# Kernel optimization log

Measured on AMD Instinct MI355X. Metric: run time of the kernel, lower is better.

## Reference

```python
import jax, jax.numpy as jnp
import numpy as np

N_NODES = 50000


def gcn_conv(x, edge_index, W, b, n_nodes):
    # Linear transform first (as in PyG GCNConv), then normalized aggregation
    xw = x @ W  # [N, out]
    src, dst = edge_index[0], edge_index[1]
    loops = jnp.arange(n_nodes, dtype=src.dtype)
    s = jnp.concatenate([src, loops])  # add self-loops
    d = jnp.concatenate([dst, loops])
    deg = jax.ops.segment_sum(jnp.ones_like(s, dtype=xw.dtype), d, num_segments=n_nodes)
    dinv = jnp.where(deg > 0, jax.lax.rsqrt(deg), 0.0)
    norm = dinv[s] * dinv[d]  # [E+N]
    msg = xw[s] * norm[:, None]  # gather + scale
    out = jax.ops.segment_sum(msg, d, num_segments=n_nodes)  # scatter-add
    return out + b


def setup_inputs() -> dict:
    key = jax.random.key(0)
    k1, k2, k3, k4 = jax.random.split(key, 4)
    in_dim, hidden = 128, 128
    n_edges = 625000
    x = jax.random.normal(k1, (N_NODES, in_dim), dtype=jnp.float32)
    edge_index = jax.random.randint(k2, (2, n_edges), 0, N_NODES, dtype=jnp.int64)
    # glorot-ish scale
    W1 = jax.random.normal(k3, (in_dim, hidden), dtype=jnp.float32) * (1.0 / np.sqrt(in_dim))
    b1 = jnp.zeros((hidden,), dtype=jnp.float32)
    W2 = jax.random.normal(k4, (hidden, hidden), dtype=jnp.float32) * (1.0 / np.sqrt(hidden))
    b2 = jnp.zeros((hidden,), dtype=jnp.float32)
    return {"x": x, "edge_index": edge_index, "W1": W1, "b1": b1, "W2": W2, "b2": b2}


def reference(x, edge_index, W1, b1, W2, b2):
    n = x.shape[0]
    h = gcn_conv(x, edge_index, W1, b1, n)
    h = jax.nn.relu(h)
    # dropout(p=0.3) is identity in eval mode
    h = gcn_conv(h, edge_index, W2, b2, n)
    return jax.nn.relu(h)
```

## Files before the change

kernel.cpp:

```cpp
#include <hip/hip_runtime.h>
#include <hip/hip_bf16.h>

#define NNODES 50000
#define BKT 64
#define LP 136
#define NXCD 8
#define NPX 6250

typedef short bf16x8 __attribute__((ext_vector_type(8)));
typedef float f32x4 __attribute__((ext_vector_type(4)));

__device__ __forceinline__ unsigned short f2bf_rn(float f) {
    unsigned int u = __float_as_uint(f);
    return (unsigned short)((u + 0x7fffu + ((u >> 16) & 1u)) >> 16);
}
__device__ __forceinline__ float bf_lo(unsigned int u) { return __uint_as_float(u << 16); }
__device__ __forceinline__ float bf_hi(unsigned int u) { return __uint_as_float(u & 0xffff0000u); }


__global__ __launch_bounds__(256) void k_wt(const float* __restrict__ W1,
                                            const float* __restrict__ W2,
                                            unsigned short* __restrict__ WT1,
                                            unsigned short* __restrict__ WT2,
                                            int* __restrict__ cnt, int N) {
    __shared__ float tile[128 * 129];
    int b = blockIdx.x, t = threadIdx.x;
    if (b < 2) {
        const float* W = b ? W2 : W1;
        unsigned short* WT = b ? WT2 : WT1;
        for (int idx = t; idx < 128 * 128; idx += 256)
            tile[(idx >> 7) * 129 + (idx & 127)] = W[idx];
        __syncthreads();
        for (int idx = t; idx < 128 * 128; idx += 256) {
            int c = idx >> 7, k = idx & 127;
            WT[c * 128 + k] = f2bf_rn(tile[k * 129 + c]);
        }
    } else {
        int i = (b - 2) * 256 + t;
        if (i < N) cnt[i] = 0;
    }
}


__device__ __forceinline__ void gather_accum(const unsigned int* __restrict__ xwb,
                                             const int* __restrict__ cnt,
                                             const unsigned short* __restrict__ bp,
                                             int degc, int lane,
                                             float& ax, float& ay) {
    float px = 0.f, py = 0.f;
    int j = 0;
    for (; j + 8 <= degc; j += 8) {
        int4 q = *(const int4*)&bp[j];
        int s0 = q.x & 0xffff, s1 = (int)((unsigned)q.x >> 16);
        int s2 = q.y & 0xffff, s3 = (int)((unsigned)q.y >> 16);
        int s4 = q.z & 0xffff, s5 = (int)((unsigned)q.z >> 16);
        int s6 = q.w & 0xffff, s7 = (int)((unsigned)q.w >> 16);
        unsigned int u0 = xwb[(size_t)s0 * 64 + lane];
        unsigned int u1 = xwb[(size_t)s1 * 64 + lane];
        unsigned int u2 = xwb[(size_t)s2 * 64 + lane];
        unsigned int u3 = xwb[(size_t)s3 * 64 + lane];
        unsigned int u4 = xwb[(size_t)s4 * 64 + lane];
        unsigned int u5 = xwb[(size_t)s5 * 64 + lane];
        unsigned int u6 = xwb[(size_t)s6 * 64 + lane];
        unsigned int u7 = xwb[(size_t)s7 * 64 + lane];
        float w0 = rsqrtf((float)cnt[s0] + 1.0f), w1 = rsqrtf((float)cnt[s1] + 1.0f);
        float w2 = rsqrtf((float)cnt[s2] + 1.0f), w3 = rsqrtf((float)cnt[s3] + 1.0f);
        float w4 = rsqrtf((float)cnt[s4] + 1.0f), w5 = rsqrtf((float)cnt[s5] + 1.0f);
        float w6 = rsqrtf((float)cnt[s6] + 1.0f), w7 = rsqrtf((float)cnt[s7] + 1.0f);
        ax = fmaf(bf_lo(u0), w0, ax);  ay = fmaf(bf_hi(u0), w0, ay);
        px = fmaf(bf_lo(u1), w1, px);  py = fmaf(bf_hi(u1), w1, py);
        ax = fmaf(bf_lo(u2), w2, ax);  ay = fmaf(bf_hi(u2), w2, ay);
        px = fmaf(bf_lo(u3), w3, px);  py = fmaf(bf_hi(u3), w3, py);
        ax = fmaf(bf_lo(u4), w4, ax);  ay = fmaf(bf_hi(u4), w4, ay);
        px = fmaf(bf_lo(u5), w5, px);  py = fmaf(bf_hi(u5), w5, py);
        ax = fmaf(bf_lo(u6), w6, ax);  ay = fmaf(bf_hi(u6), w6, ay);
        px = fmaf(bf_lo(u7), w7, px);  py = fmaf(bf_hi(u7), w7, py);
    }
    if (j + 4 <= degc) {
        int2 q = *(const int2*)&bp[j];
        int s0 = q.x & 0xffff, s1 = (int)((unsigned)q.x >> 16);
        int s2 = q.y & 0xffff, s3 = (int)((unsigned)q.y >> 16);
        unsigned int u0 = xwb[(size_t)s0 * 64 + lane];
        unsigned int u1 = xwb[(size_t)s1 * 64 + lane];
        unsigned int u2 = xwb[(size_t)s2 * 64 + lane];
        unsigned int u3 = xwb[(size_t)s3 * 64 + lane];
        float w0 = rsqrtf((float)cnt[s0] + 1.0f), w1 = rsqrtf((float)cnt[s1] + 1.0f);
        float w2 = rsqrtf((float)cnt[s2] + 1.0f), w3 = rsqrtf((float)cnt[s3] + 1.0f);
        ax = fmaf(bf_lo(u0), w0, ax);  ay = fmaf(bf_hi(u0), w0, ay);
        px = fmaf(bf_lo(u1), w1, px);  py = fmaf(bf_hi(u1), w1, py);
        ax = fmaf(bf_lo(u2), w2, ax);  ay = fmaf(bf_hi(u2), w2, ay);
        px = fmaf(bf_lo(u3), w3, px);  py = fmaf(bf_hi(u3), w3, py);
        j += 4;
    }
    for (; j < degc; ++j) {
        int s = bp[j];
        float wv = rsqrtf((float)cnt[s] + 1.0f);
        unsigned int u = xwb[(size_t)s * 64 + lane];
        ax = fmaf(bf_lo(u), wv, ax);
        ay = fmaf(bf_hi(u), wv, ay);
    }
    ax += px;
    ay += py;
}


__global__ __launch_bounds__(256) void k_gemmbucket(const float* __restrict__ X,
                                                    const unsigned short* __restrict__ WT,
                                                    unsigned short* __restrict__ Yb, int n,
                                                    const int* __restrict__ src,
                                                    const int* __restrict__ dst,
                                                    int* __restrict__ cnt,
                                                    unsigned short* __restrict__ bkt,
                                                    int E, int EBTOT) {
    __shared__ unsigned short Ep[64 * LP];
    int t = threadIdx.x;
    if ((int)blockIdx.x < EBTOT) {
        int g = blockIdx.x & (NXCD - 1);
        int kk = blockIdx.x >> 3;
        int lo = g * NPX;
        int SLOTS = E >> 2;
        int idx = kk * 256 + t;
        if (idx < SLOTS) {
            int4 d4 = ((const int4*)dst)[idx];
            int e0 = idx << 2;
            if ((unsigned)(d4.x - lo) < (unsigned)NPX) {
                int pos = atomicAdd(&cnt[d4.x], 1);
                if (pos < BKT) bkt[(size_t)d4.x * BKT + pos] = (unsigned short)src[e0];
            }
            if ((unsigned)(d4.y - lo) < (unsigned)NPX) {
                int pos = atomicAdd(&cnt[d4.y], 1);
                if (pos < BKT) bkt[(size_t)d4.y * BKT + pos] = (unsigned short)src[e0 + 1];
            }
            if ((unsigned)(d4.z - lo) < (unsigned)NPX) {
                int pos = atomicAdd(&cnt[d4.z], 1);
                if (pos < BKT) bkt[(size_t)d4.z * BKT + pos] = (unsigned short)src[e0 + 2];
            }
            if ((unsigned)(d4.w - lo) < (unsigned)NPX) {
                int pos = atomicAdd(&cnt[d4.w], 1);
                if (pos < BKT) bkt[(size_t)d4.w * BKT + pos] = (unsigned short)src[e0 + 3];
            }
        }
        if (kk == 0 && t < (E & 3)) {
            int e = (E & ~3) + t;
            int d = dst[e];
            if ((unsigned)(d - lo) < (unsigned)NPX) {
                int pos = atomicAdd(&cnt[d], 1);
                if (pos < BKT) bkt[(size_t)d * BKT + pos] = (unsigned short)src[e];
            }
        }
        return;
    }
    int gb = blockIdx.x - EBTOT;
    int lane = t & 63, w = t >> 6;
    int m = lane & 15, quad = lane >> 4;
    int base = gb * 64 + w * 16;
    int row = min(base + m, n - 1);

    bf16x8 a[4];
#pragma unroll
    for (int kt = 0; kt < 4; ++kt) {
        const float* pa = &X[(size_t)row * 128 + kt * 32 + quad * 8];
        float4 v0 = *(const float4*)pa;
        float4 v1 = *(const float4*)(pa + 4);
        a[kt][0] = (short)f2bf_rn(v0.x); a[kt][1] = (short)f2bf_rn(v0.y);
        a[kt][2] = (short)f2bf_rn(v0.z); a[kt][3] = (short)f2bf_rn(v0.w);
        a[kt][4] = (short)f2bf_rn(v1.x); a[kt][5] = (short)f2bf_rn(v1.y);
        a[kt][6] = (short)f2bf_rn(v1.z); a[kt][7] = (short)f2bf_rn(v1.w);
    }

    f32x4 acc[8];
#pragma unroll
    for (int i = 0; i < 8; ++i) acc[i] = f32x4{0.f, 0.f, 0.f, 0.f};
#pragma unroll
    for (int kt = 0; kt < 4; ++kt) {
        int ko = kt * 32 + quad * 8;
#pragma unroll
        for (int ct = 0; ct < 8; ++ct) {
            bf16x8 b = *(const bf16x8*)&WT[(ct * 16 + m) * 128 + ko];
            acc[ct] = __builtin_amdgcn_mfma_f32_16x16x32_bf16(a[kt], b, acc[ct], 0, 0, 0);
        }
    }

    unsigned short* ep = &Ep[w * 16 * LP];
#pragma unroll
    for (int ct = 0; ct < 8; ++ct)
#pragma unroll
        for (int r = 0; r < 4; ++r)
            ep[(quad * 4 + r) * LP + ct * 16 + m] = f2bf_rn(acc[ct][r]);
    __syncthreads();
    int rr = lane & 15, cc = lane >> 4;
    int orow = base + rr;
    if (orow < n) {
#pragma unroll
        for (int i2 = 0; i2 < 4; ++i2)
            ((uint4*)&Yb[(size_t)orow * 128])[cc * 4 + i2] =
                *(const uint4*)&ep[rr * LP + (cc * 4 + i2) * 8];
    }
}


__global__ __launch_bounds__(1024, 2) void k_aggemm(const unsigned int* __restrict__ xw1,
                                                    const int* __restrict__ cnt,
                                                    const unsigned short* __restrict__ bkt,
                                                    const float* __restrict__ bias,
                                                    const unsigned short* __restrict__ WT2,
                                                    unsigned short* __restrict__ xw2, int n) {
    __shared__ unsigned short Wl[128 * LP];
    __shared__ unsigned short At[16 * LP];
    int t = threadIdx.x, lane = t & 63, w = t >> 6;
    int base = blockIdx.x * 16;

    for (int idx = t; idx < 128 * 16; idx += 1024) {
        int r = idx >> 4, c8 = (idx & 15) << 3;
        *(uint4*)&Wl[r * LP + c8] = *(const uint4*)&WT2[r * 128 + c8];
    }

    int i = min(base + w, n - 1);
    int deg = cnt[i];
    int degc = min(deg, BKT);
    float di = rsqrtf((float)deg + 1.0f);
    unsigned int v0 = xw1[(size_t)i * 64 + lane];
    float ax = di * bf_lo(v0), ay = di * bf_hi(v0);
    gather_accum(xw1, cnt, &bkt[(size_t)i * BKT], degc, lane, ax, ay);
    float bx = bias[lane * 2], by = bias[lane * 2 + 1];
    ax = fmaxf(fmaf(di, ax, bx), 0.0f);
    ay = fmaxf(fmaf(di, ay, by), 0.0f);
    ((unsigned int*)&At[w * LP])[lane] = (unsigned)f2bf_rn(ax) | ((unsigned)f2bf_rn(ay) << 16);
    __syncthreads();

    int m = lane & 15, quad = lane >> 4;
    f32x4 acc = f32x4{0.f, 0.f, 0.f, 0.f};
    if (w < 8) {
        bf16x8 a[4];
#pragma unroll
        for (int kt = 0; kt < 4; ++kt)
            a[kt] = *(const bf16x8*)&At[m * LP + kt * 32 + quad * 8];
#pragma unroll
        for (int kt = 0; kt < 4; ++kt) {
            bf16x8 b = *(const bf16x8*)&Wl[(w * 16 + m) * LP + kt * 32 + quad * 8];
            acc = __builtin_amdgcn_mfma_f32_16x16x32_bf16(a[kt], b, acc, 0, 0, 0);
        }
    }
    __syncthreads();
    if (w < 8) {
#pragma unroll
        for (int r = 0; r < 4; ++r)
            At[(quad * 4 + r) * LP + w * 16 + m] = f2bf_rn(acc[r]);
    }
    __syncthreads();
    if (t < 256) {
        int row = t >> 4, q = t & 15;
        int orow = base + row;
        if (orow < n)
            *(uint4*)&xw2[(size_t)orow * 128 + q * 8] = *(const uint4*)&At[row * LP + q * 8];
    }
}


__global__ __launch_bounds__(256) void k_agg(const unsigned int* __restrict__ xwb,
                                             const int* __restrict__ cnt,
                                             const unsigned short* __restrict__ bkt,
                                             const float* __restrict__ bias,
                                             float* __restrict__ out, int n) {
    int lane = threadIdx.x & 63;
    int i = (blockIdx.x * 256 + threadIdx.x) >> 6;
    if (i >= n) return;
    int deg = cnt[i];
    int degc = min(deg, BKT);
    float di = rsqrtf((float)deg + 1.0f);
    unsigned int v0 = xwb[(size_t)i * 64 + lane];
    float ax = di * bf_lo(v0), ay = di * bf_hi(v0);
    gather_accum(xwb, cnt, &bkt[(size_t)i * BKT], degc, lane, ax, ay);
    float bx = bias[lane * 2], by = bias[lane * 2 + 1];
    ax = fmaxf(fmaf(di, ax, bx), 0.0f);
    ay = fmaxf(fmaf(di, ay, by), 0.0f);
    ((float2*)out)[(size_t)i * 64 + lane] = make_float2(ax, ay);
}


extern "C" void kernel_launch(void* const* d_in, const int* in_sizes, int n_in,
                              void* d_out, int out_size, void* d_ws, size_t ws_size,
                              hipStream_t stream) {
    const float* x  = (const float*)d_in[0];
    const int*   ei = (const int*)d_in[1];
    const float* W1 = (const float*)d_in[2];
    const float* b1 = (const float*)d_in[3];
    const float* W2 = (const float*)d_in[4];
    const float* b2 = (const float*)d_in[5];
    float* out = (float*)d_out;

    const int N = NNODES;
    const int E = in_sizes[1] / 2;
    const int* src = ei;
    const int* dst = ei + E;

    char* p = (char*)d_ws;
    size_t off = 0;
    auto take = [&](size_t bytes) -> void* {
        void* r = p + off;
        off = (off + bytes + 255) & ~(size_t)255;
        return r;
    };
    int* cnt = (int*)take((size_t)N * 4);
    unsigned short* bkt = (unsigned short*)take((size_t)N * BKT * 2);
    unsigned short* w1t = (unsigned short*)take(128 * 128 * 2);
    unsigned short* w2t = (unsigned short*)take(128 * 128 * 2);
    unsigned short* xw1 = (unsigned short*)take((size_t)N * 128 * 2);
    unsigned short* xw2 = (unsigned short*)take((size_t)N * 128 * 2);

    const int NB = (N + 255) / 256;
    const int SLOTS = E / 4;
    const int NBG = (SLOTS + 255) / 256;
    const int EBTOT = NBG * NXCD;
    const int GB = (N + 63) / 64;

    k_wt<<<2 + NB, 256, 0, stream>>>(W1, W2, w1t, w2t, cnt, N);
    k_gemmbucket<<<EBTOT + GB, 256, 0, stream>>>(x, w1t, xw1, N, src, dst, cnt, bkt, E, EBTOT);
    k_aggemm<<<(N + 15) / 16, 1024, 0, stream>>>((const unsigned int*)xw1, cnt, bkt,
                                                 b1, w2t, xw2, N);
    k_agg<<<(N * 64 + 255) / 256, 256, 0, stream>>>((const unsigned int*)xw2, cnt, bkt,
                                                    b2, out, N);
}
```

Measured before the change: 209.9 us.

## Prescale layer-2 features by source norm, persistent agg loops, simpler edge bucketing

Edge bucketing no longer filters by XCD node range. Each bucketing block now handles 8 edges per thread with vector loads and is interleaved 1-in-3 with GEMM blocks. The layer-1 aggregate+GEMM kernel becomes a persistent grid-stride loop that reads W2 straight from global memory instead of staging it in LDS, and it multiplies outputs by the row's dinv. Because xw2 is prescaled by source degree norm, the final aggregation does plain sums without per-neighbour cnt loads and rsqrt, and runs as a persistent grid. This removes dependent cnt gathers in layer 2 and the per-block W2 LDS staging, at the cost of more atomic contention across XCDs and W2 reloads from cache.

```diff
diff --git a/kernel.cpp b/kernel.cpp
--- a/kernel.cpp
+++ b/kernel.cpp
@@ -4,8 +4,9 @@
 #define NNODES 50000
 #define BKT 64
 #define LP 136
-#define NXCD 8
-#define NPX 6250
+#define EPT 8
+#define AGG_BLOCKS 2048
+#define AGE_BLOCKS 512
 
 typedef short bf16x8 __attribute__((ext_vector_type(8)));
 typedef float f32x4 __attribute__((ext_vector_type(4)));
@@ -104,6 +105,60 @@
 }
 
 
+__device__ __forceinline__ void gather_sum(const unsigned int* __restrict__ xwb,
+                                           const unsigned short* __restrict__ bp,
+                                           int degc, int lane,
+                                           float& ax, float& ay) {
+    float px = 0.f, py = 0.f;
+    int j = 0;
+    for (; j + 8 <= degc; j += 8) {
+        int4 q = *(const int4*)&bp[j];
+        int s0 = q.x & 0xffff, s1 = (int)((unsigned)q.x >> 16);
+        int s2 = q.y & 0xffff, s3 = (int)((unsigned)q.y >> 16);
+        int s4 = q.z & 0xffff, s5 = (int)((unsigned)q.z >> 16);
+        int s6 = q.w & 0xffff, s7 = (int)((unsigned)q.w >> 16);
+        unsigned int u0 = xwb[(size_t)s0 * 64 + lane];
+        unsigned int u1 = xwb[(size_t)s1 * 64 + lane];
+        unsigned int u2 = xwb[(size_t)s2 * 64 + lane];
+        unsigned int u3 = xwb[(size_t)s3 * 64 + lane];
+        unsigned int u4 = xwb[(size_t)s4 * 64 + lane];
+        unsigned int u5 = xwb[(size_t)s5 * 64 + lane];
+        unsigned int u6 = xwb[(size_t)s6 * 64 + lane];
+        unsigned int u7 = xwb[(size_t)s7 * 64 + lane];
+        ax += bf_lo(u0);  ay += bf_hi(u0);
+        px += bf_lo(u1);  py += bf_hi(u1);
+        ax += bf_lo(u2);  ay += bf_hi(u2);
+        px += bf_lo(u3);  py += bf_hi(u3);
+        ax += bf_lo(u4);  ay += bf_hi(u4);
+        px += bf_lo(u5);  py += bf_hi(u5);
+        ax += bf_lo(u6);  ay += bf_hi(u6);
+        px += bf_lo(u7);  py += bf_hi(u7);
+    }
+    if (j + 4 <= degc) {
+        int2 q = *(const int2*)&bp[j];
+        int s0 = q.x & 0xffff, s1 = (int)((unsigned)q.x >> 16);
+        int s2 = q.y & 0xffff, s3 = (int)((unsigned)q.y >> 16);
+        unsigned int u0 = xwb[(size_t)s0 * 64 + lane];
+        unsigned int u1 = xwb[(size_t)s1 * 64 + lane];
+        unsigned int u2 = xwb[(size_t)s2 * 64 + lane];
+        unsigned int u3 = xwb[(size_t)s3 * 64 + lane];
+        ax += bf_lo(u0);  ay += bf_hi(u0);
+        px += bf_lo(u1);  py += bf_hi(u1);
+        ax += bf_lo(u2);  ay += bf_hi(u2);
+        px += bf_lo(u3);  py += bf_hi(u3);
+        j += 4;
+    }
+    for (; j < degc; ++j) {
+        int s = bp[j];
+        unsigned int u = xwb[(size_t)s * 64 + lane];
+        ax += bf_lo(u);
+        ay += bf_hi(u);
+    }
+    ax += px;
+    ay += py;
+}
+
+
 __global__ __launch_bounds__(256) void k_gemmbucket(const float* __restrict__ X,
                                                     const unsigned short* __restrict__ WT,
                                                     unsigned short* __restrict__ Yb, int n,
@@ -111,46 +166,42 @@
                                                     const int* __restrict__ dst,
                                                     int* __restrict__ cnt,
                                                     unsigned short* __restrict__ bkt,
-                                                    int E, int EBTOT) {
+                                                    int E, int EB8) {
     __shared__ unsigned short Ep[64 * LP];
     int t = threadIdx.x;
-    if ((int)blockIdx.x < EBTOT) {
-        int g = blockIdx.x & (NXCD - 1);
-        int kk = blockIdx.x >> 3;
-        int lo = g * NPX;
-        int SLOTS = E >> 2;
-        int idx = kk * 256 + t;
-        if (idx < SLOTS) {
-            int4 d4 = ((const int4*)dst)[idx];
-            int e0 = idx << 2;
-            if ((unsigned)(d4.x - lo) < (unsigned)NPX) {
-                int pos = atomicAdd(&cnt[d4.x], 1);
-                if (pos < BKT) bkt[(size_t)d4.x * BKT + pos] = (unsigned short)src[e0];
+    int b = blockIdx.x;
+    int region = EB8 * 3;
+    if (b < region && (b % 3) == 0) {
+        int bid = b / 3;
+        int e0 = bid * 256 * EPT + t * EPT;
+        if (e0 + EPT <= E) {
+            int4 sa = *(const int4*)&src[e0];
+            int4 sb = *(const int4*)&src[e0 + 4];
+            int4 da = *(const int4*)&dst[e0];
+            int4 db = *(const int4*)&dst[e0 + 4];
+            int p;
+            p = atomicAdd(&cnt[da.x], 1); if (p < BKT) bkt[(size_t)da.x * BKT + p] = (unsigned short)sa.x;
+            p = atomicAdd(&cnt[da.y], 1); if (p < BKT) bkt[(size_t)da.y * BKT + p] = (unsigned short)sa.y;
+            p = atomicAdd(&cnt[da.z], 1); if (p < BKT) bkt[(size_t)da.z * BKT + p] = (unsigned short)sa.z;
+            p = atomicAdd(&cnt[da.w], 1); if (p < BKT) bkt[(size_t)da.w * BKT + p] = (unsigned short)sa.w;
+            p = atomicAdd(&cnt[db.x], 1); if (p < BKT) bkt[(size_t)db.x * BKT + p] = (unsigned short)sb.x;
+            p = atomicAdd(&cnt[db.y], 1); if (p < BKT) bkt[(size_t)db.y * BKT + p] = (unsigned short)sb.y;
+            p = atomicAdd(&cnt[db.z], 1); if (p < BKT) bkt[(size_t)db.z * BKT + p] = (unsigned short)sb.z;
+            p = atomicAdd(&cnt[db.w], 1); if (p < BKT) bkt[(size_t)db.w * BKT + p] = (unsigned short)sb.w;
+        } else {
+#pragma unroll
+            for (int k = 0; k < EPT; ++k) {
+                int e = e0 + k;
+                if (e < E) {
+                    int s = src[e], d = dst[e];
+                    int pos = atomicAdd(&cnt[d], 1);
+                    if (pos < BKT) bkt[(size_t)d * BKT + pos] = (unsigned short)s;
+                }
             }
-            if ((unsigned)(d4.y - lo) < (unsigned)NPX) {
-                int pos = atomicAdd(&cnt[d4.y], 1);
-                if (pos < BKT) bkt[(size_t)d4.y * BKT + pos] = (unsigned short)src[e0 + 1];
-            }
-            if ((unsigned)(d4.z - lo) < (unsigned)NPX) {
-                int pos = atomicAdd(&cnt[d4.z], 1);
-                if (pos < BKT) bkt[(size_t)d4.z * BKT + pos] = (unsigned short)src[e0 + 2];
-            }
-            if ((unsigned)(d4.w - lo) < (unsigned)NPX) {
-                int pos = atomicAdd(&cnt[d4.w], 1);
-                if (pos < BKT) bkt[(size_t)d4.w * BKT + pos] = (unsigned short)src[e0 + 3];
-            }
-        }
-        if (kk == 0 && t < (E & 3)) {
-            int e = (E & ~3) + t;
-            int d = dst[e];
-            if ((unsigned)(d - lo) < (unsigned)NPX) {
-                int pos = atomicAdd(&cnt[d], 1);
-                if (pos < BKT) bkt[(size_t)d * BKT + pos] = (unsigned short)src[e];
-            }
         }
         return;
     }
-    int gb = blockIdx.x - EBTOT;
+    int gb = (b < region) ? (b - (b + 2) / 3) : (b - EB8);
     int lane = t & 63, w = t >> 6;
     int m = lane & 15, quad = lane >> 4;
     int base = gb * 64 + w * 16;
@@ -176,8 +227,8 @@
         int ko = kt * 32 + quad * 8;
 #pragma unroll
         for (int ct = 0; ct < 8; ++ct) {
-            bf16x8 b = *(const bf16x8*)&WT[(ct * 16 + m) * 128 + ko];
-            acc[ct] = __builtin_amdgcn_mfma_f32_16x16x32_bf16(a[kt], b, acc[ct], 0, 0, 0);
+            bf16x8 bfrag = *(const bf16x8*)&WT[(ct * 16 + m) * 128 + ko];
+            acc[ct] = __builtin_amdgcn_mfma_f32_16x16x32_bf16(a[kt], bfrag, acc[ct], 0, 0, 0);
         }
     }
 
@@ -204,55 +255,57 @@
                                                     const unsigned short* __restrict__ bkt,
                                                     const float* __restrict__ bias,
                                                     const unsigned short* __restrict__ WT2,
-                                                    unsigned short* __restrict__ xw2, int n) {
-    __shared__ unsigned short Wl[128 * LP];
+                                                    unsigned short* __restrict__ xw2,
+                                                    int n, int ntiles) {
     __shared__ unsigned short At[16 * LP];
+    __shared__ float dis[16];
     int t = threadIdx.x, lane = t & 63, w = t >> 6;
-    int base = blockIdx.x * 16;
-
-    for (int idx = t; idx < 128 * 16; idx += 1024) {
-        int r = idx >> 4, c8 = (idx & 15) << 3;
-        *(uint4*)&Wl[r * LP + c8] = *(const uint4*)&WT2[r * 128 + c8];
-    }
-
-    int i = min(base + w, n - 1);
-    int deg = cnt[i];
-    int degc = min(deg, BKT);
-    float di = rsqrtf((float)deg + 1.0f);
-    unsigned int v0 = xw1[(size_t)i * 64 + lane];
-    float ax = di * bf_lo(v0), ay = di * bf_hi(v0);
-    gather_accum(xw1, cnt, &bkt[(size_t)i * BKT], degc, lane, ax, ay);
+    int m = lane & 15, quad = lane >> 4;
     float bx = bias[lane * 2], by = bias[lane * 2 + 1];
-    ax = fmaxf(fmaf(di, ax, bx), 0.0f);
-    ay = fmaxf(fmaf(di, ay, by), 0.0f);
-    ((unsigned int*)&At[w * LP])[lane] = (unsigned)f2bf_rn(ax) | ((unsigned)f2bf_rn(ay) << 16);
-    __syncthreads();
-
-    int m = lane & 15, quad = lane >> 4;
-    f32x4 acc = f32x4{0.f, 0.f, 0.f, 0.f};
-    if (w < 8) {
-        bf16x8 a[4];
-#pragma unroll
-        for (int kt = 0; kt < 4; ++kt)
-            a[kt] = *(const bf16x8*)&At[m * LP + kt * 32 + quad * 8];
-#pragma unroll
-        for (int kt = 0; kt < 4; ++kt) {
-            bf16x8 b = *(const bf16x8*)&Wl[(w * 16 + m) * LP + kt * 32 + quad * 8];
-            acc = __builtin_amdgcn_mfma_f32_16x16x32_bf16(a[kt], b, acc, 0, 0, 0);
-        }
-    }
-    __syncthreads();
-    if (w < 8) {
-#pragma unroll
-        for (int r = 0; r < 4; ++r)
-            At[(quad * 4 + r) * LP + w * 16 + m] = f2bf_rn(acc[r]);
-    }
-    __syncthreads();
-    if (t < 256) {
-        int row = t >> 4, q = t & 15;
-        int orow = base + row;
-        if (orow < n)
-            *(uint4*)&xw2[(size_t)orow * 128 + q * 8] = *(const uint4*)&At[row * LP + q * 8];
+
+    for (int tile = blockIdx.x; tile < ntiles; tile += gridDim.x) {
+        int base = tile * 16;
+        int i = min(base + w, n - 1);
+        int deg = cnt[i];
+        int degc = min(deg, BKT);
+        float di = rsqrtf((float)deg + 1.0f);
+        unsigned int v0 = xw1[(size_t)i * 64 + lane];
+        float ax = di * bf_lo(v0), ay = di * bf_hi(v0);
+        gather_accum(xw1, cnt, &bkt[(size_t)i * BKT], degc, lane, ax, ay);
+        ax = fmaxf(fmaf(di, ax, bx), 0.0f);
+        ay = fmaxf(fmaf(di, ay, by), 0.0f);
+        ((unsigned int*)&At[w * LP])[lane] =
+            (unsigned)f2bf_rn(ax) | ((unsigned)f2bf_rn(ay) << 16);
+        if (lane == 0) dis[w] = di;
+        __syncthreads();
+
+        f32x4 acc = f32x4{0.f, 0.f, 0.f, 0.f};
+        if (w < 8) {
+            bf16x8 a[4];
+#pragma unroll
+            for (int kt = 0; kt < 4; ++kt)
+                a[kt] = *(const bf16x8*)&At[m * LP + kt * 32 + quad * 8];
+#pragma unroll
+            for (int kt = 0; kt < 4; ++kt) {
+                bf16x8 bfrag = *(const bf16x8*)&WT2[(w * 16 + m) * 128 + kt * 32 + quad * 8];
+                acc = __builtin_amdgcn_mfma_f32_16x16x32_bf16(a[kt], bfrag, acc, 0, 0, 0);
+            }
+        }
+        __syncthreads();
+        if (w < 8) {
+#pragma unroll
+            for (int r = 0; r < 4; ++r)
+                At[(quad * 4 + r) * LP + w * 16 + m] = f2bf_rn(acc[r] * dis[quad * 4 + r]);
+        }
+        __syncthreads();
+        if (t < 256) {
+            int row = t >> 4, q = t & 15;
+            int orow = base + row;
+            if (orow < n)
+                *(uint4*)&xw2[(size_t)orow * 128 + q * 8] =
+                    *(const uint4*)&At[row * LP + q * 8];
+        }
+        __syncthreads();
     }
 }
 
@@ -263,18 +316,20 @@
                                              const float* __restrict__ bias,
                                              float* __restrict__ out, int n) {
     int lane = threadIdx.x & 63;
-    int i = (blockIdx.x * 256 + threadIdx.x) >> 6;
-    if (i >= n) return;
-    int deg = cnt[i];
-    int degc = min(deg, BKT);
-    float di = rsqrtf((float)deg + 1.0f);
-    unsigned int v0 = xwb[(size_t)i * 64 + lane];
-    float ax = di * bf_lo(v0), ay = di * bf_hi(v0);
-    gather_accum(xwb, cnt, &bkt[(size_t)i * BKT], degc, lane, ax, ay);
+    int gw = (blockIdx.x * 256 + threadIdx.x) >> 6;
+    int nw = (gridDim.x * 256) >> 6;
     float bx = bias[lane * 2], by = bias[lane * 2 + 1];
-    ax = fmaxf(fmaf(di, ax, bx), 0.0f);
-    ay = fmaxf(fmaf(di, ay, by), 0.0f);
-    ((float2*)out)[(size_t)i * 64 + lane] = make_float2(ax, ay);
+    for (int i = gw; i < n; i += nw) {
+        int deg = cnt[i];
+        int degc = min(deg, BKT);
+        float di = rsqrtf((float)deg + 1.0f);
+        unsigned int v0 = xwb[(size_t)i * 64 + lane];
+        float ax = bf_lo(v0), ay = bf_hi(v0);
+        gather_sum(xwb, &bkt[(size_t)i * BKT], degc, lane, ax, ay);
+        ax = fmaxf(fmaf(di, ax, bx), 0.0f);
+        ay = fmaxf(fmaf(di, ay, by), 0.0f);
+        ((float2*)out)[(size_t)i * 64 + lane] = make_float2(ax, ay);
+    }
 }
 
 
@@ -309,15 +364,14 @@
     unsigned short* xw2 = (unsigned short*)take((size_t)N * 128 * 2);
 
     const int NB = (N + 255) / 256;
-    const int SLOTS = E / 4;
-    const int NBG = (SLOTS + 255) / 256;
-    const int EBTOT = NBG * NXCD;
+    const int EB8 = (E + 256 * EPT - 1) / (256 * EPT);
     const int GB = (N + 63) / 64;
+    const int NT = (N + 15) / 16;
 
     k_wt<<<2 + NB, 256, 0, stream>>>(W1, W2, w1t, w2t, cnt, N);
-    k_gemmbucket<<<EBTOT + GB, 256, 0, stream>>>(x, w1t, xw1, N, src, dst, cnt, bkt, E, EBTOT);
-    k_aggemm<<<(N + 15) / 16, 1024, 0, stream>>>((const unsigned int*)xw1, cnt, bkt,
-                                                 b1, w2t, xw2, N);
-    k_agg<<<(N * 64 + 255) / 256, 256, 0, stream>>>((const unsigned int*)xw2, cnt, bkt,
-                                                    b2, out, N);
-}
+    k_gemmbucket<<<EB8 + GB, 256, 0, stream>>>(x, w1t, xw1, N, src, dst, cnt, bkt, E, EB8);
+    k_aggemm<<<AGE_BLOCKS, 1024, 0, stream>>>((const unsigned int*)xw1, cnt, bkt,
+                                              b1, w2t, xw2, N, NT);
+    k_agg<<<AGG_BLOCKS, 256, 0, stream>>>((const unsigned int*)xw2, cnt, bkt,
+                                          b2, out, N);
+}
```

After: 219.4 us. 4.6% more time.
